# Optimization experiments

Measured on AMD Instinct MI355X. Metric: run time of the kernel, lower is better.

The kernel has to match this reference:

```python
import jax, jax.numpy as jnp
import numpy as np

# Config (matches init_kwargs)
HIDDEN = 1280
NUM_EXPERTS = 16
NUM_SHARED = 2
NUM_ROUTED = NUM_EXPERTS - NUM_SHARED          # 14
TOPK = 6 - NUM_SHARED                           # num_activated - num_shared = 4
INTERMED = int(int(HIDDEN * 4.0) * 0.25)        # 1280
B, S = 2, 2048


def setup_inputs() -> dict:
    key = jax.random.key(0)
    ks = jax.random.split(key, 12)
    sc = 0.02
    x = jax.random.normal(ks[0], (B, S, HIDDEN), dtype=jnp.float32)
    # shared experts, stacked over expert axis
    W1s = jax.random.normal(ks[1], (NUM_SHARED, HIDDEN, INTERMED), dtype=jnp.float32) * sc
    b1s = jnp.zeros((NUM_SHARED, INTERMED), dtype=jnp.float32)
    W2s = jax.random.normal(ks[2], (NUM_SHARED, INTERMED, HIDDEN), dtype=jnp.float32) * sc
    b2s = jnp.zeros((NUM_SHARED, HIDDEN), dtype=jnp.float32)
    # routed experts
    W1r = jax.random.normal(ks[3], (NUM_ROUTED, HIDDEN, INTERMED), dtype=jnp.float32) * sc
    b1r = jnp.zeros((NUM_ROUTED, INTERMED), dtype=jnp.float32)
    W2r = jax.random.normal(ks[4], (NUM_ROUTED, INTERMED, HIDDEN), dtype=jnp.float32) * sc
    b2r = jnp.zeros((NUM_ROUTED, HIDDEN), dtype=jnp.float32)
    # router
    Wr = jax.random.normal(ks[5], (HIDDEN, NUM_ROUTED), dtype=jnp.float32) * sc
    br = jnp.zeros((NUM_ROUTED,), dtype=jnp.float32)
    return {"x": x, "W1s": W1s, "b1s": b1s, "W2s": W2s, "b2s": b2s,
            "W1r": W1r, "b1r": b1r, "W2r": W2r, "b2r": b2r, "Wr": Wr, "br": br}


def _gelu(x):
    return jax.nn.gelu(x, approximate=False)  # torch nn.GELU default is exact erf


def reference(x, W1s, b1s, W2s, b2s, W1r, b1r, W2r, b2r, Wr, br):
    # shared experts: sum_e FFN_e(x)
    hs = _gelu(jnp.einsum('bsh,ehi->ebsi', x, W1s) + b1s[:, None, None, :])
    shared_out = jnp.einsum('ebsi,eih->bsh', hs, W2s) + b2s.sum(0)

    # router: softmax + top-k gates scattered back to dense [B,S,E]
    logits = jnp.einsum('bsh,he->bse', x, Wr) + br
    aff = jax.nn.softmax(logits, axis=-1)
    topk_vals, topk_idx = jax.lax.top_k(aff, TOPK)
    gates = (jax.nn.one_hot(topk_idx, NUM_ROUTED, dtype=aff.dtype)
             * topk_vals[..., None]).sum(axis=-2)  # [B,S,E]

    # naive dense dispatch: every routed expert over all tokens, gate-weighted
    hr = _gelu(jnp.einsum('bsh,ehi->ebsi', x, W1r) + b1r[:, None, None, :])
    expert_out = jnp.einsum('ebsi,eih->ebsh', hr, W2r) + b2r[:, None, None, :]
    routed_out = jnp.einsum('bse,ebsh->bsh', gates, expert_out)

    return shared_out + routed_out + x
```

## Files before the change

### kernel.cpp

```cpp
#include <hip/hip_runtime.h>
#include <hip/hip_bf16.h>
#include <math.h>

#define H      1280
#define NE     16
#define NR     14
#define TK     4
#define T      4096
#define NROWS  24576
#define MAXT   112

typedef __bf16 bf16x8 __attribute__((ext_vector_type(8)));
typedef float  f32x4  __attribute__((ext_vector_type(4)));
typedef unsigned short us8 __attribute__((ext_vector_type(8)));

__device__ __forceinline__ unsigned short f2bf(float f) {
  unsigned int u = __float_as_uint(f);
  u += 0x7fffu + ((u >> 16) & 1u);
  return (unsigned short)(u >> 16);
}
__device__ __forceinline__ float bf2f(unsigned short u) {
  return __uint_as_float(((unsigned int)u) << 16);
}

__device__ __forceinline__ void gll16(const unsigned short* g, unsigned short* l) {
  __builtin_amdgcn_global_load_lds(
      (const __attribute__((address_space(1))) void*)g,
      (__attribute__((address_space(3))) void*)l, 16, 0, 0);
}

__global__ void k_init(int* cnt, int* fill) {
  int i = threadIdx.x;
  if (i < 16) { cnt[i] = 0; fill[i] = 0; }
}

__global__ void k_cast_x(const float* __restrict__ x, unsigned short* __restrict__ xb) {
  int i = blockIdx.x * 256 + threadIdx.x;
  float4 v = reinterpret_cast<const float4*>(x)[i];
  ushort4 b;
  b.x = f2bf(v.x); b.y = f2bf(v.y); b.z = f2bf(v.z); b.w = f2bf(v.w);
  reinterpret_cast<ushort4*>(xb)[i] = b;
}

__global__ void k_transpose(const float* __restrict__ W1s, const float* __restrict__ W2s,
                            const float* __restrict__ W1r, const float* __restrict__ W2r,
                            unsigned short* __restrict__ w1b, unsigned short* __restrict__ w2b) {
  int mat = blockIdx.z;
  int fam = mat >> 4;
  int e   = mat & 15;
  size_t msz = (size_t)H * H;
  const float* src;
  unsigned short* dst;
  if (fam == 0) {
    src = (e < 2) ? W1s + (size_t)e * msz : W1r + (size_t)(e - 2) * msz;
    dst = w1b + (size_t)e * msz;
  } else {
    src = (e < 2) ? W2s + (size_t)e * msz : W2r + (size_t)(e - 2) * msz;
    dst = w2b + (size_t)e * msz;
  }
  __shared__ unsigned short tile[64][72];
  int tx = threadIdx.x & 15;
  int ty = threadIdx.x >> 4;
  int bx = blockIdx.x * 64;
  int by = blockIdx.y * 64;
#pragma unroll
  for (int p = 0; p < 4; p++) {
    int r = p * 16 + ty;
    float4 v = *reinterpret_cast<const float4*>(&src[(size_t)(by + r) * H + bx + tx * 4]);
    tile[tx * 4 + 0][r] = f2bf(v.x);
    tile[tx * 4 + 1][r] = f2bf(v.y);
    tile[tx * 4 + 2][r] = f2bf(v.z);
    tile[tx * 4 + 3][r] = f2bf(v.w);
  }
  __syncthreads();
  int tx8 = threadIdx.x & 7;
  int rr  = threadIdx.x >> 3;
#pragma unroll
  for (int p = 0; p < 2; p++) {
    int n = p * 32 + rr;
    us8 o = *reinterpret_cast<const us8*>(&tile[n][tx8 * 8]);
    *reinterpret_cast<us8*>(&dst[(size_t)(bx + n) * H + by + tx8 * 8]) = o;
  }
}

__global__ void k_router(const float* __restrict__ x, const float* __restrict__ Wr,
                         const float* __restrict__ br,
                         int* __restrict__ topk_e, float* __restrict__ topk_g) {
  int t  = blockIdx.x * 4 + (threadIdx.x >> 6);
  int ln = threadIdx.x & 63;
  float part[NR];
#pragma unroll
  for (int e = 0; e < NR; e++) part[e] = 0.f;
  const float* xr = x + (size_t)t * H;
  for (int k = ln; k < H; k += 64) {
    float xv = xr[k];
    const float* w = Wr + (size_t)k * NR;
#pragma unroll
    for (int e = 0; e < NR; e++) part[e] += xv * w[e];
  }
  float aff[NR];
#pragma unroll
  for (int e = 0; e < NR; e++) {
    float v = part[e];
#pragma unroll
    for (int off = 32; off; off >>= 1) v += __shfl_down(v, off);
    aff[e] = v + br[e];
  }
  if (ln == 0) {
    float mx = aff[0];
#pragma unroll
    for (int e = 1; e < NR; e++) mx = fmaxf(mx, aff[e]);
    float p[NR]; float s = 0.f;
#pragma unroll
    for (int e = 0; e < NR; e++) { p[e] = expf(aff[e] - mx); s += p[e]; }
    float inv = 1.f / s;
    unsigned used = 0;
    for (int j = 0; j < TK; j++) {
      int be = -1; float bv = -1.f;
#pragma unroll
      for (int e = 0; e < NR; e++)
        if (!((used >> e) & 1u) && p[e] > bv) { bv = p[e]; be = e; }
      used |= 1u << be;
      topk_e[t * TK + j] = be;
      topk_g[t * TK + j] = bv * inv;
    }
  }
}

__global__ void k_count(const int* __restrict__ topk_e, int* __restrict__ cnt) {
  __shared__ int hist[NR];
  int tid = threadIdx.x;
  if (tid < NR) hist[tid] = 0;
  __syncthreads();
  int t = blockIdx.x * 256 + tid;
#pragma unroll
  for (int j = 0; j < TK; j++)
    atomicAdd(&hist[topk_e[t * TK + j]], 1);
  __syncthreads();
  if (tid < NR) atomicAdd(&cnt[tid], hist[tid]);
}

__global__ void k_prefix(const int* __restrict__ cnt, int* __restrict__ segbase,
                         int* __restrict__ segcnt, int* __restrict__ tile_seg,
                         int* __restrict__ tile_m0) {
  if (threadIdx.x == 0) {
    int sc[NE];
    sc[0] = T; sc[1] = T;
    for (int e = 0; e < NR; e++) sc[2 + e] = cnt[e];
    int b = 0;
    for (int s = 0; s < NE; s++) { segbase[s] = b; segcnt[s] = sc[s]; b += sc[s]; }
    int nt = 0;
    for (int s = 0; s < NE; s++)
      for (int m = 0; m < sc[s]; m += 256) { tile_seg[nt] = s; tile_m0[nt] = m; nt++; }
    for (int i = nt; i < MAXT; i++) { tile_seg[i] = -1; tile_m0[i] = 0; }
  }
}

__global__ void k_fill(const int* __restrict__ topk_e,
                       const int* __restrict__ segbase, int* __restrict__ fill,
                       int* __restrict__ rowtok, int* __restrict__ tokrow) {
  __shared__ int lhist[NR];
  __shared__ int lbase[NR];
  int tid = threadIdx.x;
  if (tid < NR) lhist[tid] = 0;
  __syncthreads();
  int t = blockIdx.x * 256 + tid;
  rowtok[t]     = t;
  rowtok[T + t] = t;
  int e[TK], off[TK];
#pragma unroll
  for (int j = 0; j < TK; j++) {
    e[j]   = topk_e[t * TK + j];
    off[j] = atomicAdd(&lhist[e[j]], 1);
  }
  __syncthreads();
  if (tid < NR) lbase[tid] = atomicAdd(&fill[tid], lhist[tid]);
  __syncthreads();
#pragma unroll
  for (int j = 0; j < TK; j++) {
    int r = segbase[2 + e[j]] + lbase[e[j]] + off[j];
    rowtok[r] = t;
    tokrow[t * TK + j] = r;
  }
}


__global__ __launch_bounds__(512, 2) void k_gemm1(
    const unsigned short* __restrict__ xb, const unsigned short* __restrict__ w1b,
    const float* __restrict__ b1s, const float* __restrict__ b1r,
    const int* __restrict__ rowtok, const int* __restrict__ segbase,
    const int* __restrict__ segcnt, const int* __restrict__ tile_seg,
    const int* __restrict__ tile_m0, unsigned short* __restrict__ hbuf) {
  int seg = tile_seg[blockIdx.y];
  if (seg < 0) return;
  int m0  = tile_m0[blockIdx.y];
  int cnt = segcnt[seg];
  int n0  = blockIdx.x * 256;
  int sb  = segbase[seg];
  const unsigned short* Bw = w1b + (size_t)seg * H * H;
  const float* bias = (seg < 2) ? b1s + (size_t)seg * H : b1r + (size_t)(seg - 2) * H;

  __shared__ __align__(16) unsigned short Al[256 * 64];
  __shared__ __align__(16) unsigned short Bl[256 * 64];

  int tid = threadIdx.x;
  int wv = tid >> 6, ln = tid & 63;
  int rw = (wv & 1) * 128, cw = (wv >> 1) * 64;
  int quad = ln >> 4, l16 = ln & 15;
  int lrow = tid >> 3;
  int ldst = (tid & 7) * 8;
  int lkc  = (((tid & 7) ^ (lrow & 7))) * 8;

  const unsigned short* asrc[4];
  const unsigned short* bsrc[4];
#pragma unroll
  for (int p = 0; p < 4; p++) {
    int row = p * 64 + lrow;
    int gm  = m0 + row;
    int tok = (gm < cnt) ? rowtok[sb + gm] : 0;
    asrc[p] = xb + (size_t)tok * H + lkc;
    bsrc[p] = Bw + (size_t)(n0 + row) * H + lkc;
  }

  int xsw = (quad ^ (l16 & 7)) * 8;

  f32x4 acc[8][4];
#pragma unroll
  for (int i = 0; i < 8; i++)
#pragma unroll
    for (int j = 0; j < 4; j++) acc[i][j] = (f32x4){0.f, 0.f, 0.f, 0.f};

  for (int k0 = 0; k0 < H; k0 += 64) {
    __syncthreads();
#pragma unroll
    for (int p = 0; p < 4; p++) {
      int row = p * 64 + lrow;
      gll16(asrc[p] + k0, &Al[row * 64 + ldst]);
      gll16(bsrc[p] + k0, &Bl[row * 64 + ldst]);
    }
    __syncthreads();
#pragma unroll
    for (int kk = 0; kk < 64; kk += 32) {
      bf16x8 af[8], bfr[4];
#pragma unroll
      for (int i = 0; i < 8; i++)
        af[i] = *reinterpret_cast<const bf16x8*>(&Al[(rw + i * 16 + l16) * 64 + (xsw ^ kk)]);
#pragma unroll
      for (int j = 0; j < 4; j++)
        bfr[j] = *reinterpret_cast<const bf16x8*>(&Bl[(cw + j * 16 + l16) * 64 + (xsw ^ kk)]);
#pragma unroll
      for (int i = 0; i < 8; i++)
#pragma unroll
        for (int j = 0; j < 4; j++)
          acc[i][j] = __builtin_amdgcn_mfma_f32_16x16x32_bf16(af[i], bfr[j], acc[i][j], 0, 0, 0);
    }
  }

#pragma unroll
  for (int i = 0; i < 8; i++) {
#pragma unroll
    for (int r = 0; r < 4; r++) {
      int m = m0 + rw + i * 16 + quad * 4 + r;
      if (m >= cnt) continue;
      size_t ro = (size_t)(sb + m) * H;
#pragma unroll
      for (int j = 0; j < 4; j++) {
        int n = n0 + cw + j * 16 + l16;
        float v = acc[i][j][r] + bias[n];
        float g = 0.5f * v * (1.f + erff(v * 0.70710678118654752f));
        hbuf[ro + n] = f2bf(g);
      }
    }
  }
}

__global__ __launch_bounds__(512, 2) void k_gemm2(
    const unsigned short* __restrict__ hbuf, const unsigned short* __restrict__ w2b,
    const float* __restrict__ b2s, const float* __restrict__ b2r,
    const int* __restrict__ segbase, const int* __restrict__ segcnt,
    const int* __restrict__ tile_seg, const int* __restrict__ tile_m0,
    unsigned short* __restrict__ rbuf) {
  int seg = tile_seg[blockIdx.y];
  if (seg < 0) return;
  int m0  = tile_m0[blockIdx.y];
  int cnt = segcnt[seg];
  int n0  = blockIdx.x * 256;
  int sb  = segbase[seg];
  const unsigned short* Bw = w2b + (size_t)seg * H * H;
  const float* bias = (seg < 2) ? b2s + (size_t)seg * H : b2r + (size_t)(seg - 2) * H;

  __shared__ __align__(16) unsigned short Al[256 * 64];
  __shared__ __align__(16) unsigned short Bl[256 * 64];

  int tid = threadIdx.x;
  int wv = tid >> 6, ln = tid & 63;
  int rw = (wv & 1) * 128, cw = (wv >> 1) * 64;
  int quad = ln >> 4, l16 = ln & 15;
  int lrow = tid >> 3;
  int ldst = (tid & 7) * 8;
  int lkc  = (((tid & 7) ^ (lrow & 7))) * 8;

  const unsigned short* asrc[4];
  const unsigned short* bsrc[4];
#pragma unroll
  for (int p = 0; p < 4; p++) {
    int row = p * 64 + lrow;
    int ar  = sb + m0 + row;
    if (ar >= NROWS) ar = 0;
    asrc[p] = hbuf + (size_t)ar * H + lkc;
    bsrc[p] = Bw + (size_t)(n0 + row) * H + lkc;
  }

  int xsw = (quad ^ (l16 & 7)) * 8;

  f32x4 acc[8][4];
#pragma unroll
  for (int i = 0; i < 8; i++)
#pragma unroll
    for (int j = 0; j < 4; j++) acc[i][j] = (f32x4){0.f, 0.f, 0.f, 0.f};

  for (int k0 = 0; k0 < H; k0 += 64) {
    __syncthreads();
#pragma unroll
    for (int p = 0; p < 4; p++) {
      int row = p * 64 + lrow;
      gll16(asrc[p] + k0, &Al[row * 64 + ldst]);
      gll16(bsrc[p] + k0, &Bl[row * 64 + ldst]);
    }
    __syncthreads();
#pragma unroll
    for (int kk = 0; kk < 64; kk += 32) {
      bf16x8 af[8], bfr[4];
#pragma unroll
      for (int i = 0; i < 8; i++)
        af[i] = *reinterpret_cast<const bf16x8*>(&Al[(rw + i * 16 + l16) * 64 + (xsw ^ kk)]);
#pragma unroll
      for (int j = 0; j < 4; j++)
        bfr[j] = *reinterpret_cast<const bf16x8*>(&Bl[(cw + j * 16 + l16) * 64 + (xsw ^ kk)]);
#pragma unroll
      for (int i = 0; i < 8; i++)
#pragma unroll
        for (int j = 0; j < 4; j++)
          acc[i][j] = __builtin_amdgcn_mfma_f32_16x16x32_bf16(af[i], bfr[j], acc[i][j], 0, 0, 0);
    }
  }

#pragma unroll
  for (int i = 0; i < 8; i++) {
#pragma unroll
    for (int r = 0; r < 4; r++) {
      int m = m0 + rw + i * 16 + quad * 4 + r;
      if (m >= cnt) continue;
      size_t ro = (size_t)(sb + m) * H;
#pragma unroll
      for (int j = 0; j < 4; j++) {
        int n = n0 + cw + j * 16 + l16;
        rbuf[ro + n] = f2bf(acc[i][j][r] + bias[n]);
      }
    }
  }
}

__global__ void k_combine(const float* __restrict__ x, const unsigned short* __restrict__ rbuf,
                          const int* __restrict__ tokrow, const float* __restrict__ topk_g,
                          float* __restrict__ out) {
  int i = blockIdx.x * 256 + threadIdx.x;
  int t = i / (H / 4);
  int c = (i - t * (H / 4)) * 4;
  size_t xo = (size_t)t * H + c;
  float4 acc = *reinterpret_cast<const float4*>(&x[xo]);
  {
    ushort4 u0 = *reinterpret_cast<const ushort4*>(&rbuf[(size_t)t * H + c]);
    ushort4 u1 = *reinterpret_cast<const ushort4*>(&rbuf[(size_t)(T + t) * H + c]);
    acc.x += bf2f(u0.x) + bf2f(u1.x);
    acc.y += bf2f(u0.y) + bf2f(u1.y);
    acc.z += bf2f(u0.z) + bf2f(u1.z);
    acc.w += bf2f(u0.w) + bf2f(u1.w);
  }
#pragma unroll
  for (int j = 0; j < TK; j++) {
    int r   = tokrow[t * TK + j];
    float g = topk_g[t * TK + j];
    ushort4 u = *reinterpret_cast<const ushort4*>(&rbuf[(size_t)r * H + c]);
    acc.x += g * bf2f(u.x);
    acc.y += g * bf2f(u.y);
    acc.z += g * bf2f(u.z);
    acc.w += g * bf2f(u.w);
  }
  *reinterpret_cast<float4*>(&out[xo]) = acc;
}

extern "C" void kernel_launch(void* const* d_in, const int* in_sizes, int n_in,
                              void* d_out, int out_size, void* d_ws, size_t ws_size,
                              hipStream_t stream) {
  const float* x   = (const float*)d_in[0];
  const float* W1s = (const float*)d_in[1];
  const float* b1s = (const float*)d_in[2];
  const float* W2s = (const float*)d_in[3];
  const float* b2s = (const float*)d_in[4];
  const float* W1r = (const float*)d_in[5];
  const float* b1r = (const float*)d_in[6];
  const float* W2r = (const float*)d_in[7];
  const float* b2r = (const float*)d_in[8];
  const float* Wr  = (const float*)d_in[9];
  const float* br  = (const float*)d_in[10];
  float* out = (float*)d_out;

  char* ws = (char*)d_ws;
  const size_t SZ_XB = (size_t)T * H * 2;
  const size_t SZ_WB = (size_t)NE * H * H * 2;
  const size_t SZ_H  = (size_t)NROWS * H * 2;
  size_t off = 0;
  unsigned short* xb   = (unsigned short*)(ws + off); off += SZ_XB;
  unsigned short* w1b  = (unsigned short*)(ws + off); off += SZ_WB;
  unsigned short* w2b  = (unsigned short*)(ws + off); off += SZ_WB;
  unsigned short* hbuf = (unsigned short*)(ws + off); off += SZ_H;
  int*   rowtok  = (int*)(ws + off);   off += NROWS * 4;
  int*   tokrow  = (int*)(ws + off);   off += T * TK * 4;
  int*   topk_e  = (int*)(ws + off);   off += T * TK * 4;
  float* topk_g  = (float*)(ws + off); off += T * TK * 4;
  int*   cnt     = (int*)(ws + off);   off += 64;
  int*   fill    = (int*)(ws + off);   off += 64;
  int*   segbase = (int*)(ws + off);   off += 64;
  int*   segcnt  = (int*)(ws + off);   off += 64;
  int*   tile_seg = (int*)(ws + off);  off += MAXT * 4;
  int*   tile_m0  = (int*)(ws + off);  off += MAXT * 4;
  unsigned short* rbuf = (unsigned short*)ws;

  hipLaunchKernelGGL(k_init, dim3(1), dim3(64), 0, stream, cnt, fill);
  hipLaunchKernelGGL(k_cast_x, dim3((T * H / 4) / 256), dim3(256), 0, stream, x, xb);
  hipLaunchKernelGGL(k_transpose, dim3(20, 20, 32), dim3(256), 0, stream,
                     W1s, W2s, W1r, W2r, w1b, w2b);
  hipLaunchKernelGGL(k_router, dim3(T / 4), dim3(256), 0, stream, x, Wr, br, topk_e, topk_g);
  hipLaunchKernelGGL(k_count, dim3(T / 256), dim3(256), 0, stream, topk_e, cnt);
  hipLaunchKernelGGL(k_prefix, dim3(1), dim3(1), 0, stream, cnt, segbase, segcnt, tile_seg, tile_m0);
  hipLaunchKernelGGL(k_fill, dim3(T / 256), dim3(256), 0, stream,
                     topk_e, segbase, fill, rowtok, tokrow);
  hipLaunchKernelGGL(k_gemm1, dim3(5, MAXT, 1), dim3(512), 0, stream,
                     xb, w1b, b1s, b1r, rowtok, segbase, segcnt, tile_seg, tile_m0, hbuf);
  hipLaunchKernelGGL(k_gemm2, dim3(5, MAXT, 1), dim3(512), 0, stream,
                     hbuf, w2b, b2s, b2r, segbase, segcnt, tile_seg, tile_m0, rbuf);
  hipLaunchKernelGGL(k_combine, dim3((T * H / 4) / 256), dim3(256), 0, stream,
                     x, rbuf, tokrow, topk_g, out);
}
```

Baseline: 609.8 us.

## Double-buffer LDS in MoE GEMMs with prefetch and phased MFMA scheduling

Merges the two expert GEMM kernels into one template and double-buffers the A/B LDS tiles. The next k-tile is prefetched via global_load_lds while the current one is computed, using explicit vmcnt waits and raw s_barrier instead of two __syncthreads per tile. The MFMA work is split into four quadrant phases, each with its own fragment loads and s_setprio raised around the MFMAs, to interleave LDS reads with matrix math. LDS use doubles to 128KB per block, which likely cuts residency from two blocks per CU to one, and each k-tile now has five barriers.

```diff
diff --git a/kernel.cpp b/kernel.cpp
--- a/kernel.cpp
+++ b/kernel.cpp
@@ -9,6 +9,7 @@
 #define T      4096
 #define NROWS  24576
 #define MAXT   112
+#define NT     (H / 64)
 
 typedef __bf16 bf16x8 __attribute__((ext_vector_type(8)));
 typedef float  f32x4  __attribute__((ext_vector_type(4)));
@@ -185,23 +186,26 @@
 }
 
 
-__global__ __launch_bounds__(512, 2) void k_gemm1(
-    const unsigned short* __restrict__ xb, const unsigned short* __restrict__ w1b,
-    const float* __restrict__ b1s, const float* __restrict__ b1r,
-    const int* __restrict__ rowtok, const int* __restrict__ segbase,
-    const int* __restrict__ segcnt, const int* __restrict__ tile_seg,
-    const int* __restrict__ tile_m0, unsigned short* __restrict__ hbuf) {
+template<int MODE>
+__global__ __launch_bounds__(512, 2) void k_gemm(
+    const unsigned short* __restrict__ Abase,
+    const unsigned short* __restrict__ Wb,
+    const float* __restrict__ bs, const float* __restrict__ brr,
+    const int* __restrict__ rowtok,
+    const int* __restrict__ segbase, const int* __restrict__ segcnt,
+    const int* __restrict__ tile_seg, const int* __restrict__ tile_m0,
+    unsigned short* __restrict__ obuf) {
   int seg = tile_seg[blockIdx.y];
   if (seg < 0) return;
   int m0  = tile_m0[blockIdx.y];
   int cnt = segcnt[seg];
   int n0  = blockIdx.x * 256;
   int sb  = segbase[seg];
-  const unsigned short* Bw = w1b + (size_t)seg * H * H;
-  const float* bias = (seg < 2) ? b1s + (size_t)seg * H : b1r + (size_t)(seg - 2) * H;
-
-  __shared__ __align__(16) unsigned short Al[256 * 64];
-  __shared__ __align__(16) unsigned short Bl[256 * 64];
+  const unsigned short* Bw = Wb + (size_t)seg * H * H;
+  const float* bias = (seg < 2) ? bs + (size_t)seg * H : brr + (size_t)(seg - 2) * H;
+
+  __shared__ __align__(16) unsigned short Al[2][256 * 64];
+  __shared__ __align__(16) unsigned short Bl[2][256 * 64];
 
   int tid = threadIdx.x;
   int wv = tid >> 6, ln = tid & 63;
@@ -216,9 +220,15 @@
 #pragma unroll
   for (int p = 0; p < 4; p++) {
     int row = p * 64 + lrow;
-    int gm  = m0 + row;
-    int tok = (gm < cnt) ? rowtok[sb + gm] : 0;
-    asrc[p] = xb + (size_t)tok * H + lkc;
+    if (MODE == 0) {
+      int gm  = m0 + row;
+      int tok = (gm < cnt) ? rowtok[sb + gm] : 0;
+      asrc[p] = Abase + (size_t)tok * H + lkc;
+    } else {
+      int ar = sb + m0 + row;
+      if (ar >= NROWS) ar = 0;
+      asrc[p] = Abase + (size_t)ar * H + lkc;
+    }
     bsrc[p] = Bw + (size_t)(n0 + row) * H + lkc;
   }
 
@@ -230,30 +240,110 @@
 #pragma unroll
     for (int j = 0; j < 4; j++) acc[i][j] = (f32x4){0.f, 0.f, 0.f, 0.f};
 
-  for (int k0 = 0; k0 < H; k0 += 64) {
-    __syncthreads();
+  auto STAGE = [&](int tt) {
+    int kb = tt << 6;
+    int bf = tt & 1;
 #pragma unroll
     for (int p = 0; p < 4; p++) {
       int row = p * 64 + lrow;
-      gll16(asrc[p] + k0, &Al[row * 64 + ldst]);
-      gll16(bsrc[p] + k0, &Bl[row * 64 + ldst]);
+      gll16(asrc[p] + kb, &Al[bf][row * 64 + ldst]);
+      gll16(bsrc[p] + kb, &Bl[bf][row * 64 + ldst]);
     }
-    __syncthreads();
-#pragma unroll
-    for (int kk = 0; kk < 64; kk += 32) {
-      bf16x8 af[8], bfr[4];
-#pragma unroll
-      for (int i = 0; i < 8; i++)
-        af[i] = *reinterpret_cast<const bf16x8*>(&Al[(rw + i * 16 + l16) * 64 + (xsw ^ kk)]);
-#pragma unroll
-      for (int j = 0; j < 4; j++)
-        bfr[j] = *reinterpret_cast<const bf16x8*>(&Bl[(cw + j * 16 + l16) * 64 + (xsw ^ kk)]);
-#pragma unroll
-      for (int i = 0; i < 8; i++)
-#pragma unroll
-        for (int j = 0; j < 4; j++)
-          acc[i][j] = __builtin_amdgcn_mfma_f32_16x16x32_bf16(af[i], bfr[j], acc[i][j], 0, 0, 0);
+  };
+
+  STAGE(0);
+
+  bf16x8 a0[4][2], a1[4][2], b0[2][2], b1[2][2];
+
+#pragma unroll 2
+  for (int t = 0; t < NT; ++t) {
+    const int cb = t & 1;
+    if (t + 1 < NT) {
+      STAGE(t + 1);
+      asm volatile("s_waitcnt vmcnt(8)" ::: "memory");
+    } else {
+      asm volatile("s_waitcnt vmcnt(0)" ::: "memory");
     }
+    __builtin_amdgcn_sched_barrier(0);
+    asm volatile("s_barrier" ::: "memory");
+
+#pragma unroll
+    for (int i = 0; i < 4; i++)
+#pragma unroll
+      for (int kk = 0; kk < 2; kk++)
+        a0[i][kk] = *reinterpret_cast<const bf16x8*>(
+            &Al[cb][(rw + i * 16 + l16) * 64 + (xsw ^ (kk << 5))]);
+#pragma unroll
+    for (int j = 0; j < 2; j++)
+#pragma unroll
+      for (int kk = 0; kk < 2; kk++)
+        b0[j][kk] = *reinterpret_cast<const bf16x8*>(
+            &Bl[cb][(cw + j * 16 + l16) * 64 + (xsw ^ (kk << 5))]);
+    __builtin_amdgcn_s_setprio(1);
+#pragma unroll
+    for (int kk = 0; kk < 2; kk++)
+#pragma unroll
+      for (int i = 0; i < 4; i++)
+#pragma unroll
+        for (int j = 0; j < 2; j++)
+          acc[i][j] = __builtin_amdgcn_mfma_f32_16x16x32_bf16(a0[i][kk], b0[j][kk], acc[i][j], 0, 0, 0);
+    __builtin_amdgcn_s_setprio(0);
+    asm volatile("s_waitcnt lgkmcnt(0)" ::: "memory");
+    asm volatile("s_barrier" ::: "memory");
+
+#pragma unroll
+    for (int j = 0; j < 2; j++)
+#pragma unroll
+      for (int kk = 0; kk < 2; kk++)
+        b1[j][kk] = *reinterpret_cast<const bf16x8*>(
+            &Bl[cb][(cw + (j + 2) * 16 + l16) * 64 + (xsw ^ (kk << 5))]);
+    __builtin_amdgcn_s_setprio(1);
+#pragma unroll
+    for (int kk = 0; kk < 2; kk++)
+#pragma unroll
+      for (int i = 0; i < 4; i++)
+#pragma unroll
+        for (int j = 0; j < 2; j++)
+          acc[i][j + 2] = __builtin_amdgcn_mfma_f32_16x16x32_bf16(a0[i][kk], b1[j][kk], acc[i][j + 2], 0, 0, 0);
+    __builtin_amdgcn_s_setprio(0);
+    asm volatile("s_waitcnt lgkmcnt(0)" ::: "memory");
+    asm volatile("s_barrier" ::: "memory");
+
+#pragma unroll
+    for (int i = 0; i < 4; i++)
+#pragma unroll
+      for (int kk = 0; kk < 2; kk++)
+        a1[i][kk] = *reinterpret_cast<const bf16x8*>(
+            &Al[cb][(rw + (i + 4) * 16 + l16) * 64 + (xsw ^ (kk << 5))]);
+    __builtin_amdgcn_s_setprio(1);
+#pragma unroll
+    for (int kk = 0; kk < 2; kk++)
+#pragma unroll
+      for (int i = 0; i < 4; i++)
+#pragma unroll
+        for (int j = 0; j < 2; j++)
+          acc[i + 4][j + 2] = __builtin_amdgcn_mfma_f32_16x16x32_bf16(a1[i][kk], b1[j][kk], acc[i + 4][j + 2], 0, 0, 0);
+    __builtin_amdgcn_s_setprio(0);
+    asm volatile("s_waitcnt lgkmcnt(0)" ::: "memory");
+    asm volatile("s_barrier" ::: "memory");
+
+#pragma unroll
+    for (int j = 0; j < 2; j++)
+#pragma unroll
+      for (int kk = 0; kk < 2; kk++)
+        b0[j][kk] = *reinterpret_cast<const bf16x8*>(
+            &Bl[cb][(cw + j * 16 + l16) * 64 + (xsw ^ (kk << 5))]);
+    __builtin_amdgcn_s_setprio(1);
+#pragma unroll
+    for (int kk = 0; kk < 2; kk++)
+#pragma unroll
+      for (int i = 0; i < 4; i++)
+#pragma unroll
+        for (int j = 0; j < 2; j++)
+          acc[i + 4][j] = __builtin_amdgcn_mfma_f32_16x16x32_bf16(a1[i][kk], b0[j][kk], acc[i + 4][j], 0, 0, 0);
+    __builtin_amdgcn_s_setprio(0);
+    asm volatile("s_waitcnt lgkmcnt(0)" ::: "memory");
+    asm volatile("s_barrier" ::: "memory");
   }
 
 #pragma unroll
@@ -267,95 +357,12 @@
       for (int j = 0; j < 4; j++) {
         int n = n0 + cw + j * 16 + l16;
         float v = acc[i][j][r] + bias[n];
-        float g = 0.5f * v * (1.f + erff(v * 0.70710678118654752f));
-        hbuf[ro + n] = f2bf(g);
-      }
-    }
-  }
-}
-
-__global__ __launch_bounds__(512, 2) void k_gemm2(
-    const unsigned short* __restrict__ hbuf, const unsigned short* __restrict__ w2b,
-    const float* __restrict__ b2s, const float* __restrict__ b2r,
-    const int* __restrict__ segbase, const int* __restrict__ segcnt,
-    const int* __restrict__ tile_seg, const int* __restrict__ tile_m0,
-    unsigned short* __restrict__ rbuf) {
-  int seg = tile_seg[blockIdx.y];
-  if (seg < 0) return;
-  int m0  = tile_m0[blockIdx.y];
-  int cnt = segcnt[seg];
-  int n0  = blockIdx.x * 256;
-  int sb  = segbase[seg];
-  const unsigned short* Bw = w2b + (size_t)seg * H * H;
-  const float* bias = (seg < 2) ? b2s + (size_t)seg * H : b2r + (size_t)(seg - 2) * H;
-
-  __shared__ __align__(16) unsigned short Al[256 * 64];
-  __shared__ __align__(16) unsigned short Bl[256 * 64];
-
-  int tid = threadIdx.x;
-  int wv = tid >> 6, ln = tid & 63;
-  int rw = (wv & 1) * 128, cw = (wv >> 1) * 64;
-  int quad = ln >> 4, l16 = ln & 15;
-  int lrow = tid >> 3;
-  int ldst = (tid & 7) * 8;
-  int lkc  = (((tid & 7) ^ (lrow & 7))) * 8;
-
-  const unsigned short* asrc[4];
-  const unsigned short* bsrc[4];
-#pragma unroll
-  for (int p = 0; p < 4; p++) {
-    int row = p * 64 + lrow;
-    int ar  = sb + m0 + row;
-    if (ar >= NROWS) ar = 0;
-    asrc[p] = hbuf + (size_t)ar * H + lkc;
-    bsrc[p] = Bw + (size_t)(n0 + row) * H + lkc;
-  }
-
-  int xsw = (quad ^ (l16 & 7)) * 8;
-
-  f32x4 acc[8][4];
-#pragma unroll
-  for (int i = 0; i < 8; i++)
-#pragma unroll
-    for (int j = 0; j < 4; j++) acc[i][j] = (f32x4){0.f, 0.f, 0.f, 0.f};
-
-  for (int k0 = 0; k0 < H; k0 += 64) {
-    __syncthreads();
-#pragma unroll
-    for (int p = 0; p < 4; p++) {
-      int row = p * 64 + lrow;
-      gll16(asrc[p] + k0, &Al[row * 64 + ldst]);
-      gll16(bsrc[p] + k0, &Bl[row * 64 + ldst]);
-    }
-    __syncthreads();
-#pragma unroll
-    for (int kk = 0; kk < 64; kk += 32) {
-      bf16x8 af[8], bfr[4];
-#pragma unroll
-      for (int i = 0; i < 8; i++)
-        af[i] = *reinterpret_cast<const bf16x8*>(&Al[(rw + i * 16 + l16) * 64 + (xsw ^ kk)]);
-#pragma unroll
-      for (int j = 0; j < 4; j++)
-        bfr[j] = *reinterpret_cast<const bf16x8*>(&Bl[(cw + j * 16 + l16) * 64 + (xsw ^ kk)]);
-#pragma unroll
-      for (int i = 0; i < 8; i++)
-#pragma unroll
-        for (int j = 0; j < 4; j++)
-          acc[i][j] = __builtin_amdgcn_mfma_f32_16x16x32_bf16(af[i], bfr[j], acc[i][j], 0, 0, 0);
-    }
-  }
-
-#pragma unroll
-  for (int i = 0; i < 8; i++) {
-#pragma unroll
-    for (int r = 0; r < 4; r++) {
-      int m = m0 + rw + i * 16 + quad * 4 + r;
-      if (m >= cnt) continue;
-      size_t ro = (size_t)(sb + m) * H;
-#pragma unroll
-      for (int j = 0; j < 4; j++) {
-        int n = n0 + cw + j * 16 + l16;
-        rbuf[ro + n] = f2bf(acc[i][j][r] + bias[n]);
+        if (MODE == 0) {
+          float g = 0.5f * v * (1.f + erff(v * 0.70710678118654752f));
+          obuf[ro + n] = f2bf(g);
+        } else {
+          obuf[ro + n] = f2bf(v);
+        }
       }
     }
   }
@@ -436,10 +443,10 @@
   hipLaunchKernelGGL(k_prefix, dim3(1), dim3(1), 0, stream, cnt, segbase, segcnt, tile_seg, tile_m0);
   hipLaunchKernelGGL(k_fill, dim3(T / 256), dim3(256), 0, stream,
                      topk_e, segbase, fill, rowtok, tokrow);
-  hipLaunchKernelGGL(k_gemm1, dim3(5, MAXT, 1), dim3(512), 0, stream,
+  hipLaunchKernelGGL(HIP_KERNEL_NAME(k_gemm<0>), dim3(5, MAXT, 1), dim3(512), 0, stream,
                      xb, w1b, b1s, b1r, rowtok, segbase, segcnt, tile_seg, tile_m0, hbuf);
-  hipLaunchKernelGGL(k_gemm2, dim3(5, MAXT, 1), dim3(512), 0, stream,
-                     hbuf, w2b, b2s, b2r, segbase, segcnt, tile_seg, tile_m0, rbuf);
+  hipLaunchKernelGGL(HIP_KERNEL_NAME(k_gemm<1>), dim3(5, MAXT, 1), dim3(512), 0, stream,
+                     hbuf, w2b, b2s, b2r, rowtok, segbase, segcnt, tile_seg, tile_m0, rbuf);
   hipLaunchKernelGGL(k_combine, dim3((T * H / 4) / 256), dim3(256), 0, stream,
                      x, rbuf, tokrow, topk_g, out);
 }
```

After: 638.1 us. 1.05x slower.
